# Optimization experiments

Measured on AMD Instinct MI355X. Metric: run time of the kernel, lower is better.

The kernel has to match this reference:

```python
import jax, jax.numpy as jnp
import numpy as np

D_MODEL = 1024
N_HEADS = 16
D_K = D_MODEL // N_HEADS
ROPE_THETA = 10000.0


def setup_inputs() -> dict:
    key = jax.random.key(0)
    ks = jax.random.split(key, 5)
    B, S = 2, 2048
    scale = 1.0 / np.sqrt(D_MODEL)
    return {
        "x": jax.random.normal(ks[0], (B, S, D_MODEL), dtype=jnp.float32),
        "token_positions": jnp.arange(S, dtype=jnp.int32),
        "Wq": jax.random.normal(ks[1], (D_MODEL, D_MODEL), dtype=jnp.float32) * scale,
        "Wk": jax.random.normal(ks[2], (D_MODEL, D_MODEL), dtype=jnp.float32) * scale,
        "Wv": jax.random.normal(ks[3], (D_MODEL, D_MODEL), dtype=jnp.float32) * scale,
        "Wo": jax.random.normal(ks[4], (D_MODEL, D_MODEL), dtype=jnp.float32) * scale,
    }


def apply_rope(x, positions):
    # x: [b, h, s, d_k]; interleaved-pair rotary embedding, theta=10000
    half = D_K // 2
    inv_freq = ROPE_THETA ** (-jnp.arange(0, half, dtype=x.dtype) * 2.0 / D_K)  # [half]
    angles = positions.astype(x.dtype)[:, None] * inv_freq[None, :]             # [s, half]
    cos, sin = jnp.cos(angles), jnp.sin(angles)                                 # [s, half]
    x1 = x[..., 0::2]
    x2 = x[..., 1::2]
    r1 = x1 * cos - x2 * sin
    r2 = x1 * sin + x2 * cos
    # re-interleave
    return jnp.stack([r1, r2], axis=-1).reshape(x.shape)


def reference(x, token_positions, Wq, Wk, Wv, Wo):
    B, S, _ = x.shape
    # Linear(d_model, d_model) with no bias: y = x @ W.T
    Q = jnp.einsum("bsd,ed->bse", x, Wq).reshape(B, S, N_HEADS, D_K).transpose(0, 2, 1, 3)
    K = jnp.einsum("bsd,ed->bse", x, Wk).reshape(B, S, N_HEADS, D_K).transpose(0, 2, 1, 3)
    V = jnp.einsum("bsd,ed->bse", x, Wv).reshape(B, S, N_HEADS, D_K).transpose(0, 2, 1, 3)
    Q = apply_rope(Q, token_positions)
    K = apply_rope(K, token_positions)
    scores = jnp.einsum("bhqd,bhkd->bhqk", Q, K) / jnp.sqrt(jnp.asarray(D_K, x.dtype))
    causal = jnp.tril(jnp.ones((S, S), dtype=bool))
    scores = jnp.where(causal[None, None, :, :], scores, jnp.asarray(-jnp.inf, x.dtype))
    attn = jax.nn.softmax(scores, axis=-1)
    out = jnp.einsum("bhqk,bhkd->bhqd", attn, V)            # [b, h, s, d_k]
    out = out.transpose(0, 2, 1, 3).reshape(B, S, D_MODEL)   # [b, s, d_model]
    return jnp.einsum("bsd,ed->bse", out, Wo)
```

## Files before the change

kernel.cpp:

```cpp
#include <hip/hip_runtime.h>
#include <hip/hip_bf16.h>
#include <math.h>

#define SEQ 2048
#define NH  16
#define DKH 64
#define DM  1024
#define MR  4096

using bf16x8 = __attribute__((ext_vector_type(8))) short;
using f32x4  = __attribute__((ext_vector_type(4))) float;
using f32x16 = __attribute__((ext_vector_type(16))) float;

__device__ __forceinline__ ushort f2b(float f) {
  unsigned u = __float_as_uint(f);
  return (ushort)((u + 0x7fffu + ((u >> 16) & 1u)) >> 16);
}

__device__ __forceinline__ float exp2_fast(float x) {
  float r; asm("v_exp_f32 %0, %1" : "=v"(r) : "v"(x)); return r;
}

__device__ __forceinline__ unsigned cvt_pk(float lo, float hi) {
  __hip_bfloat162 h = __float22bfloat162_rn(float2{lo, hi});
  return *reinterpret_cast<unsigned*>(&h);
}

__device__ __forceinline__ float xhalf_max(float x) {
  auto r = __builtin_amdgcn_permlane32_swap(__float_as_uint(x), __float_as_uint(x), false, false);
  return fmaxf(__uint_as_float(r[0]), __uint_as_float(r[1]));
}
__device__ __forceinline__ float xhalf_add(float x) {
  auto r = __builtin_amdgcn_permlane32_swap(__float_as_uint(x), __float_as_uint(x), false, false);
  return __uint_as_float(r[0]) + __uint_as_float(r[1]);
}

__device__ __forceinline__ void gll16(const void* g, void* l) {
  __builtin_amdgcn_global_load_lds(
      (const __attribute__((address_space(1))) void*)g,
      (__attribute__((address_space(3))) void*)l, 16, 0, 0);
}

__global__ __launch_bounds__(256) void cvt_all(
    const float* __restrict__ x,  const float* __restrict__ wq,
    const float* __restrict__ wk, const float* __restrict__ wv,
    const float* __restrict__ wo,
    ushort* __restrict__ xb,  ushort* __restrict__ wqb, ushort* __restrict__ wkb,
    ushort* __restrict__ wvb, ushort* __restrict__ wob)
{
  size_t e = ((size_t)blockIdx.x * 256 + threadIdx.x) * 4;
  const float* s; ushort* d; size_t off;
  if      (e < 4194304) { s = x;  d = xb;  off = e; }
  else if (e < 5242880) { s = wq; d = wqb; off = e - 4194304; }
  else if (e < 6291456) { s = wk; d = wkb; off = e - 5242880; }
  else if (e < 7340032) { s = wv; d = wvb; off = e - 6291456; }
  else                  { s = wo; d = wob; off = e - 7340032; }
  float4 f = *(const float4*)(s + off);
  ushort4 o4 = { f2b(f.x), f2b(f.y), f2b(f.z), f2b(f.w) };
  *(ushort4*)(d + off) = o4;
}

__global__ __launch_bounds__(512) void gemm_qkv(
    const ushort* __restrict__ X,
    const ushort* __restrict__ Wq, const ushort* __restrict__ Wk, const ushort* __restrict__ Wv,
    ushort* __restrict__ Q, ushort* __restrict__ K, ushort* __restrict__ Vt,
    const int* __restrict__ pos)
{
  __shared__ __align__(16) char As[2][16384];
  __shared__ __align__(16) char Bs[2][16384];

  const int id  = blockIdx.x;
  const int xcd = id & 7;
  const int i   = id >> 3;
  const int mt  = xcd * 4 + (i & 3);
  const int nt  = i >> 2;
  const int m0  = mt * 128;
  const int nG  = nt * 128;
  const int z   = nG >> 10;
  const int n0  = nG & 1023;
  const ushort* W = (z == 0) ? Wq : (z == 1) ? Wk : Wv;

  const int tid  = threadIdx.x;
  const int lane = tid & 63;
  const int w    = tid >> 6;
  const int wm   = (w >> 2) * 64;
  const int wn   = (w & 3) * 32;
  const int li   = lane & 15;
  const int g    = lane >> 4;

  f32x4 acc[4][2] = {};

  auto stage = [&](int t, int buf) {
    const int k0 = t * 64;
    #pragma unroll
    for (int it = 0; it < 2; ++it) {
      const int L  = w * 2048 + it * 1024 + lane * 16;
      const int r  = L >> 7;
      const int sc = ((L >> 4) & 7) ^ (r & 7);
      gll16(X + (size_t)(m0 + r) * DM + k0 + sc * 8, &As[buf][w * 2048 + it * 1024]);
      gll16(W + (size_t)(n0 + r) * DM + k0 + sc * 8, &Bs[buf][w * 2048 + it * 1024]);
    }
  };

  auto compute = [&](int buf) {
    #pragma unroll
    for (int ks = 0; ks < 2; ++ks) {
      bf16x8 af[4], bfr[2];
      #pragma unroll
      for (int mf = 0; mf < 4; ++mf) {
        const int row = wm + mf * 16 + li;
        af[mf] = *(const bf16x8*)(&As[buf][row * 128 + (((ks * 4 + g) ^ (row & 7)) << 4)]);
      }
      #pragma unroll
      for (int nf = 0; nf < 2; ++nf) {
        const int row = wn + nf * 16 + li;
        bfr[nf] = *(const bf16x8*)(&Bs[buf][row * 128 + (((ks * 4 + g) ^ (row & 7)) << 4)]);
      }
      #pragma unroll
      for (int mf = 0; mf < 4; ++mf)
        #pragma unroll
        for (int nf = 0; nf < 2; ++nf)
          acc[mf][nf] = __builtin_amdgcn_mfma_f32_16x16x32_bf16(af[mf], bfr[nf], acc[mf][nf], 0, 0, 0);
    }
  };

  stage(0, 0);
  for (int t = 0; t < 16; ++t) {
    if (t < 15) {
      stage(t + 1, (t + 1) & 1);
      __builtin_amdgcn_sched_barrier(0);
      asm volatile("s_waitcnt vmcnt(4)" ::: "memory");
    } else {
      asm volatile("s_waitcnt vmcnt(0)" ::: "memory");
    }
    __builtin_amdgcn_s_barrier();
    __builtin_amdgcn_sched_barrier(0);
    compute(t & 1);
    __builtin_amdgcn_sched_barrier(0);
    __builtin_amdgcn_s_barrier();
  }

  #pragma unroll
  for (int nf = 0; nf < 2; ++nf) {
    const int n = n0 + wn + nf * 16 + li;
    const int h = n >> 6;
    const int d = n & 63;
    if (z == 2) {
      #pragma unroll
      for (int mf = 0; mf < 4; ++mf) {
        const int m  = m0 + wm + mf * 16 + g * 4;
        const int b  = m >> 11;
        const int s2 = m & (SEQ - 1);
        ushort4 pk = { f2b(acc[mf][nf][0]), f2b(acc[mf][nf][1]),
                       f2b(acc[mf][nf][2]), f2b(acc[mf][nf][3]) };
        *(ushort4*)(Vt + (((size_t)b * NH + h) * DKH + d) * SEQ + s2) = pk;
      }
    } else {
      ushort* DST = (z == 0) ? Q : K;
      const float freq = __expf(-(float)(d >> 1) * 0.2878231366242557f);
      #pragma unroll
      for (int mf = 0; mf < 4; ++mf) {
        #pragma unroll
        for (int r = 0; r < 4; ++r) {
          const int m  = m0 + wm + mf * 16 + g * 4 + r;
          const int b  = m >> 11;
          const int s2 = m & (SEQ - 1);
          const float ang = (float)pos[s2] * freq;
          float sn, cs;
          __sincosf(ang, &sn, &cs);
          const float v1 = acc[mf][nf][r];
          const float v2 = __shfl_xor(v1, 1);
          float ov = (d & 1) ? (v2 * sn + v1 * cs)
                             : (v1 * cs - v2 * sn);
          if (z == 0) ov *= 0.1803368801111204f;
          DST[(((size_t)b * NH + h) * SEQ + s2) * DKH + d] = f2b(ov);
        }
      }
    }
  }
}

__global__ __launch_bounds__(512) void gemm_wo(
    const ushort* __restrict__ A, const ushort* __restrict__ W,
    float* __restrict__ out)
{
  __shared__ __align__(16) char As[2][16384];
  __shared__ __align__(16) char Bs[2][16384];

  const int id  = blockIdx.x;
  const int xcd = id & 7;
  const int i   = id >> 3;
  const int mt  = xcd * 4 + (i & 3);
  const int nt  = i >> 2;
  const int m0  = mt * 128;
  const int n0  = nt * 128;

  const int tid  = threadIdx.x;
  const int lane = tid & 63;
  const int w    = tid >> 6;
  const int wm   = (w >> 2) * 64;
  const int wn   = (w & 3) * 32;
  const int li   = lane & 15;
  const int g    = lane >> 4;

  f32x4 acc[4][2] = {};

  auto stage = [&](int t, int buf) {
    const int k0 = t * 64;
    #pragma unroll
    for (int it = 0; it < 2; ++it) {
      const int L  = w * 2048 + it * 1024 + lane * 16;
      const int r  = L >> 7;
      const int sc = ((L >> 4) & 7) ^ (r & 7);
      gll16(A + (size_t)(m0 + r) * DM + k0 + sc * 8, &As[buf][w * 2048 + it * 1024]);
      gll16(W + (size_t)(n0 + r) * DM + k0 + sc * 8, &Bs[buf][w * 2048 + it * 1024]);
    }
  };

  auto compute = [&](int buf) {
    #pragma unroll
    for (int ks = 0; ks < 2; ++ks) {
      bf16x8 af[4], bfr[2];
      #pragma unroll
      for (int mf = 0; mf < 4; ++mf) {
        const int row = wm + mf * 16 + li;
        af[mf] = *(const bf16x8*)(&As[buf][row * 128 + (((ks * 4 + g) ^ (row & 7)) << 4)]);
      }
      #pragma unroll
      for (int nf = 0; nf < 2; ++nf) {
        const int row = wn + nf * 16 + li;
        bfr[nf] = *(const bf16x8*)(&Bs[buf][row * 128 + (((ks * 4 + g) ^ (row & 7)) << 4)]);
      }
      #pragma unroll
      for (int mf = 0; mf < 4; ++mf)
        #pragma unroll
        for (int nf = 0; nf < 2; ++nf)
          acc[mf][nf] = __builtin_amdgcn_mfma_f32_16x16x32_bf16(af[mf], bfr[nf], acc[mf][nf], 0, 0, 0);
    }
  };

  stage(0, 0);
  for (int t = 0; t < 16; ++t) {
    if (t < 15) {
      stage(t + 1, (t + 1) & 1);
      __builtin_amdgcn_sched_barrier(0);
      asm volatile("s_waitcnt vmcnt(4)" ::: "memory");
    } else {
      asm volatile("s_waitcnt vmcnt(0)" ::: "memory");
    }
    __builtin_amdgcn_s_barrier();
    __builtin_amdgcn_sched_barrier(0);
    compute(t & 1);
    __builtin_amdgcn_sched_barrier(0);
    __builtin_amdgcn_s_barrier();
  }

  #pragma unroll
  for (int nf = 0; nf < 2; ++nf)
    #pragma unroll
    for (int mf = 0; mf < 4; ++mf)
      #pragma unroll
      for (int r = 0; r < 4; ++r)
        out[(size_t)(m0 + wm + mf * 16 + g * 4 + r) * DM + n0 + wn + nf * 16 + li] = acc[mf][nf][r];
}

__global__ __launch_bounds__(64) void attn(
    const ushort* __restrict__ Q, const ushort* __restrict__ K,
    const ushort* __restrict__ Vt, ushort* __restrict__ AO)
{
  __shared__ __align__(16) char Ks[8192];
  __shared__ __align__(16) char Vs[8192];

  const int lane = threadIdx.x & 63;
  const int lq   = lane & 31;
  const int hi   = lane >> 5;

  const int bx  = blockIdx.x;
  const int xcd = bx & 7;
  const int i   = bx >> 3;
  const int uu  = 63 - (i >> 2);
  const int bh  = (i & 3) * 8 + xcd;
  const int q0w = uu * 32;
  const int ntr = (uu >> 1) + 1;
  const int q_abs = q0w + lq;

  const ushort* Qb = Q  + (size_t)bh * SEQ * DKH;
  const ushort* Kb = K  + (size_t)bh * SEQ * DKH;
  const ushort* Vb = Vt + (size_t)bh * DKH * SEQ;

  bf16x8 qf[4];
  #pragma unroll
  for (int db = 0; db < 4; ++db)
    qf[db] = *(const bf16x8*)(Qb + (size_t)(q0w + lq) * DKH + db * 16 + hi * 8);

  f32x16 o0 = {}, o1 = {};
  float m_ = -INFINITY, l_ = 0.f;

  auto stage = [&](int kt) {
    const int k0 = kt * 64;
    #pragma unroll
    for (int it = 0; it < 8; ++it) {
      const int L  = it * 1024 + lane * 16;
      const int r  = L >> 7;
      const int sc = ((L >> 4) & 7) ^ (r & 7);
      gll16(Kb + (size_t)(k0 + r) * DKH + sc * 8, Ks + it * 1024);
      gll16(Vb + (size_t)r * SEQ + k0 + sc * 8,   Vs + it * 1024);
    }
  };

#define PVSTEP(P, S4) do {                                                   \
    unsigned A0 = cvt_pk((P)[((S4)&1)*8 + 0], (P)[((S4)&1)*8 + 1]);          \
    unsigned A1 = cvt_pk((P)[((S4)&1)*8 + 2], (P)[((S4)&1)*8 + 3]);          \
    unsigned B0 = cvt_pk((P)[((S4)&1)*8 + 4], (P)[((S4)&1)*8 + 5]);          \
    unsigned B1 = cvt_pk((P)[((S4)&1)*8 + 6], (P)[((S4)&1)*8 + 7]);          \
    auto r0 = __builtin_amdgcn_permlane32_swap(A0, B0, false, false);        \
    auto r1 = __builtin_amdgcn_permlane32_swap(A1, B1, false, false);        \
    int4 ti = { (int)r0[0], (int)r1[0], (int)r0[1], (int)r1[1] };            \
    bf16x8 pf = *(bf16x8*)&ti;                                               \
    const int uv = (S4) * 2 + hi;                                            \
    bf16x8 va = *(const bf16x8*)(Vs + lq * 128      + ((uv ^ (lq & 7)) << 4)); \
    bf16x8 vb = *(const bf16x8*)(Vs + (32+lq) * 128 + ((uv ^ (lq & 7)) << 4)); \
    o0 = __builtin_amdgcn_mfma_f32_32x32x16_bf16(va, pf, o0, 0, 0, 0);       \
    o1 = __builtin_amdgcn_mfma_f32_32x32x16_bf16(vb, pf, o1, 0, 0, 0);       \
  } while (0)

  auto computeT = [&](int t, bool diag) {
    const int k0 = t * 64;

    f32x16 st0 = {}, st1 = {};
    __builtin_amdgcn_s_setprio(1);
    #pragma unroll
    for (int db = 0; db < 4; ++db) {
      const int uk = db * 2 + hi;
      bf16x8 ka = *(const bf16x8*)(Ks + lq * 128      + ((uk ^ (lq & 7)) << 4));
      bf16x8 kb = *(const bf16x8*)(Ks + (32+lq) * 128 + ((uk ^ (lq & 7)) << 4));
      st0 = __builtin_amdgcn_mfma_f32_32x32x16_bf16(ka, qf[db], st0, 0, 0, 0);
      st1 = __builtin_amdgcn_mfma_f32_32x32x16_bf16(kb, qf[db], st1, 0, 0, 0);
    }
    __builtin_amdgcn_s_setprio(0);

    if (diag) {
      #pragma unroll
      for (int reg = 0; reg < 16; ++reg) {
        const int kvr = (reg & 3) + 8 * (reg >> 2) + 4 * hi;
        if (k0 + kvr > q_abs)      st0[reg] = -1e30f;
        if (k0 + 32 + kvr > q_abs) st1[reg] = -1e30f;
      }
    }

    float mx = st0[0];
    #pragma unroll
    for (int r = 1; r < 16; ++r) mx = fmaxf(mx, st0[r]);
    #pragma unroll
    for (int r = 0; r < 16; ++r) mx = fmaxf(mx, st1[r]);
    mx = xhalf_max(mx);

    const bool resc = !__all(mx - m_ <= 8.0f);
    float al = 1.0f;
    if (resc) { const float nm = fmaxf(m_, mx); al = exp2_fast(m_ - nm); m_ = nm; }

    float rs = 0.f;
    #pragma unroll
    for (int r = 0; r < 16; ++r) { st0[r] = exp2_fast(st0[r] - m_); rs += st0[r]; }
    #pragma unroll
    for (int r = 0; r < 16; ++r) { st1[r] = exp2_fast(st1[r] - m_); rs += st1[r]; }
    rs = xhalf_add(rs);

    if (resc) {
      l_ = l_ * al + rs;
      #pragma unroll
      for (int r = 0; r < 16; ++r) { o0[r] *= al; o1[r] *= al; }
    } else {
      l_ += rs;
    }

    __builtin_amdgcn_s_setprio(1);
    PVSTEP(st0, 0);
    PVSTEP(st0, 1);
    PVSTEP(st1, 2);
    PVSTEP(st1, 3);
    __builtin_amdgcn_s_setprio(0);
  };

  for (int t = 0; t < ntr; ++t) {
    __builtin_amdgcn_sched_barrier(0);
    stage(t);
    __builtin_amdgcn_sched_barrier(0);
    asm volatile("s_waitcnt vmcnt(0)" ::: "memory");
    computeT(t, t == ntr - 1);
  }

  const float inv = 1.0f / l_;
  const int b = bh >> 4, h = bh & 15;
  ushort* dst = AO + ((size_t)b * SEQ + q_abs) * DM + h * DKH;

#define STORE16(OV, DSUB) do {                                               \
    _Pragma("unroll")                                                        \
    for (int rq = 0; rq < 4; ++rq) {                                         \
      const int d0 = (DSUB) * 32 + rq * 8 + hi * 4;                          \
      uint2 pk = { cvt_pk((OV)[rq*4+0] * inv, (OV)[rq*4+1] * inv),           \
                   cvt_pk((OV)[rq*4+2] * inv, (OV)[rq*4+3] * inv) };         \
      *(uint2*)(dst + d0) = pk;                                              \
    }                                                                        \
  } while (0)

  STORE16(o0, 0);
  STORE16(o1, 1);
}

extern "C" void kernel_launch(void* const* d_in, const int* in_sizes, int n_in,
                              void* d_out, int out_size, void* d_ws, size_t ws_size,
                              hipStream_t stream)
{
  const float* x   = (const float*)d_in[0];
  const int*   pos = (const int*)  d_in[1];
  const float* Wq  = (const float*)d_in[2];
  const float* Wk  = (const float*)d_in[3];
  const float* Wv  = (const float*)d_in[4];
  const float* Wo  = (const float*)d_in[5];
  float* out = (float*)d_out;

  ushort* ws  = (ushort*)d_ws;
  ushort* xb  = ws;
  ushort* wqb = xb  + 4194304;
  ushort* wkb = wqb + 1048576;
  ushort* wvb = wkb + 1048576;
  ushort* wob = wvb + 1048576;
  ushort* Qb  = wob + 1048576;
  ushort* Kb  = Qb  + 4194304;
  ushort* Vtb = Kb  + 4194304;
  ushort* AOb = Vtb + 4194304;

  cvt_all<<<8192, 256, 0, stream>>>(x, Wq, Wk, Wv, Wo, xb, wqb, wkb, wvb, wob);
  gemm_qkv<<<768, 512, 0, stream>>>(xb, wqb, wkb, wvb, Qb, Kb, Vtb, pos);
  attn<<<2048, 64, 0, stream>>>(Qb, Kb, Vtb, AOb);
  gemm_wo<<<256, 512, 0, stream>>>(AOb, wob, out);
}
```

Measured before the change: 113.2 us.

## Split attention KV loop across four waves with LDS softmax merge

The attention kernel goes from one wave per 32-query block to four waves. Each wave handles every fourth KV tile with its own LDS staging buffers, and the partial outputs and (m, l) statistics are then merged in wave 0 using a log-sum-exp rescale. This is meant to cut the serial KV-loop latency of long causal rows and even out per-block work. In exchange it uses 64KB of LDS per block, which limits occupancy, and adds a merge step after a block-wide barrier.

Result: faster. 110.9 us (-2.0%).

```diff
diff --git a/kernel.cpp b/kernel.cpp
--- a/kernel.cpp
+++ b/kernel.cpp
@@ -264,14 +264,15 @@
         out[(size_t)(m0 + wm + mf * 16 + g * 4 + r) * DM + n0 + wn + nf * 16 + li] = acc[mf][nf][r];
 }
 
-__global__ __launch_bounds__(64) void attn(
+__global__ __launch_bounds__(256) void attn(
     const ushort* __restrict__ Q, const ushort* __restrict__ K,
     const ushort* __restrict__ Vt, ushort* __restrict__ AO)
 {
-  __shared__ __align__(16) char Ks[8192];
-  __shared__ __align__(16) char Vs[8192];
-
-  const int lane = threadIdx.x & 63;
+  __shared__ __align__(16) char smem[65536];
+
+  const int tid  = threadIdx.x;
+  const int lane = tid & 63;
+  const int w    = tid >> 6;
   const int lq   = lane & 31;
   const int hi   = lane >> 5;
 
@@ -287,6 +288,9 @@
   const ushort* Qb = Q  + (size_t)bh * SEQ * DKH;
   const ushort* Kb = K  + (size_t)bh * SEQ * DKH;
   const ushort* Vb = Vt + (size_t)bh * DKH * SEQ;
+
+  char* Ks = smem + w * 16384;
+  char* Vs = Ks + 8192;
 
   bf16x8 qf[4];
   #pragma unroll
@@ -382,7 +386,7 @@
     __builtin_amdgcn_s_setprio(0);
   };
 
-  for (int t = 0; t < ntr; ++t) {
+  for (int t = w; t < ntr; t += 4) {
     __builtin_amdgcn_sched_barrier(0);
     stage(t);
     __builtin_amdgcn_sched_barrier(0);
@@ -390,9 +394,47 @@
     computeT(t, t == ntr - 1);
   }
 
-  const float inv = 1.0f / l_;
-  const int b = bh >> 4, h = bh & 15;
-  ushort* dst = AO + ((size_t)b * SEQ + q_abs) * DM + h * DKH;
+  if (w != 0) {
+    float* Om = (float*)(smem + w * 16384);
+    #pragma unroll
+    for (int r = 0; r < 16; ++r) {
+      Om[r * 64 + lane]        = o0[r];
+      Om[(16 + r) * 64 + lane] = o1[r];
+    }
+    float* Ml = (float*)(smem + w * 16384 + 8192);
+    Ml[lane * 2 + 0] = m_;
+    Ml[lane * 2 + 1] = l_;
+  }
+  __syncthreads();
+  if (w == 0) {
+    float mw[3], lw[3];
+    float ms = m_;
+    #pragma unroll
+    for (int j = 0; j < 3; ++j) {
+      const float* Ml = (const float*)(smem + (j + 1) * 16384 + 8192);
+      mw[j] = Ml[lane * 2 + 0];
+      lw[j] = Ml[lane * 2 + 1];
+      ms = fmaxf(ms, mw[j]);
+    }
+    const float s0 = exp2_fast(m_ - ms);
+    float lt = l_ * s0;
+    #pragma unroll
+    for (int r = 0; r < 16; ++r) { o0[r] *= s0; o1[r] *= s0; }
+    #pragma unroll
+    for (int j = 0; j < 3; ++j) {
+      const float sj = exp2_fast(mw[j] - ms);
+      lt += lw[j] * sj;
+      const float* Om = (const float*)(smem + (j + 1) * 16384);
+      #pragma unroll
+      for (int r = 0; r < 16; ++r) {
+        o0[r] += Om[r * 64 + lane] * sj;
+        o1[r] += Om[(16 + r) * 64 + lane] * sj;
+      }
+    }
+
+    const float inv = 1.0f / lt;
+    const int b = bh >> 4, h = bh & 15;
+    ushort* dst = AO + ((size_t)b * SEQ + q_abs) * DM + h * DKH;
 
 #define STORE16(OV, DSUB) do {                                               \
     _Pragma("unroll")                                                        \
@@ -404,8 +446,9 @@
     }                                                                        \
   } while (0)
 
-  STORE16(o0, 0);
-  STORE16(o1, 1);
+    STORE16(o0, 0);
+    STORE16(o1, 1);
+  }
 }
 
 extern "C" void kernel_launch(void* const* d_in, const int* in_sizes, int n_in,
@@ -433,6 +476,6 @@
 
   cvt_all<<<8192, 256, 0, stream>>>(x, Wq, Wk, Wv, Wo, xb, wqb, wkb, wvb, wob);
   gemm_qkv<<<768, 512, 0, stream>>>(xb, wqb, wkb, wvb, Qb, Kb, Vtb, pos);
-  attn<<<2048, 64, 0, stream>>>(Qb, Kb, Vtb, AOb);
+  attn<<<2048, 256, 0, stream>>>(Qb, Kb, Vtb, AOb);
   gemm_wo<<<256, 512, 0, stream>>>(AOb, wob, out);
 }
```
